# Kernel tuning notes

Measured on AMD Instinct MI355X. Metric: run time of the kernel, lower is better.

Reference implementation:

```python
import jax, jax.numpy as jnp
import numpy as np

N_NODES = 20000
DIM = 128
N_EDGES = 500000
BATCH = 16384
EPS = 1e-6  # torch.nn.PairwiseDistance default eps


def setup_inputs() -> dict:
    key = jax.random.key(0)
    k = jax.random.split(key, 8)
    edges = jax.random.randint(k[0], (2, N_EDGES), 0, N_NODES, dtype=jnp.int64 if jax.config.jax_enable_x64 else jnp.int32)
    nodes_p_star = jnp.sort(jax.random.randint(k[1], (BATCH,), 0, N_NODES))
    nodes_p = jnp.sort(jax.random.randint(k[2], (BATCH,), 0, N_NODES))
    # learned parameters, init in [-1, 1) as in the torch module
    beta_p = 2.0 * jax.random.uniform(k[3], (N_NODES,), dtype=jnp.float32) - 1.0
    beta_p_star = 2.0 * jax.random.uniform(k[4], (N_NODES,), dtype=jnp.float32) - 1.0
    p = 2.0 * jax.random.uniform(k[5], (N_NODES, DIM), dtype=jnp.float32) - 1.0
    p_star = 2.0 * jax.random.uniform(k[6], (N_NODES, DIM), dtype=jnp.float32) - 1.0
    return {
        "edges": edges,
        "nodes_p_star": nodes_p_star,
        "nodes_p": nodes_p,
        "beta_p": beta_p,
        "beta_p_star": beta_p_star,
        "p": p,
        "p_star": p_star,
    }


def reference(edges, nodes_p_star, nodes_p, beta_p, beta_p_star, p, p_star):
    # ---- link term: sum over observed edges of (beta - dist) ----
    beta_pair = beta_p_star[edges[0]] + beta_p[edges[1]]  # [E]
    diff = p[edges[0]] - p_star[edges[1]]                 # [E, D]
    # torch PairwiseDistance adds eps to the difference before the norm
    z_dist = jnp.sqrt(jnp.sum((diff + EPS) ** 2, axis=-1))
    link_term = jnp.sum(beta_pair - z_dist)

    # ---- non-link term: triu-masked sum of exp(beta - cdist) ----
    bps = beta_p_star[nodes_p_star]   # [Ns]
    bp = beta_p[nodes_p]              # [Np]
    ps = p_star[nodes_p_star]         # [Ns, D]
    pp = p[nodes_p]                   # [Np, D]
    beta_mat = bps[None, :] + bp[:, None]          # [Np, Ns]
    # cdist(ps, pp) -> [Ns, Np] via Gram trick
    sq = (jnp.sum(ps * ps, axis=-1)[:, None]
          + jnp.sum(pp * pp, axis=-1)[None, :]
          - 2.0 * jnp.einsum('nd,md->nm', ps, pp))
    dist_mat = jnp.sqrt(jnp.maximum(sq, 0.0))      # [Ns, Np]
    intensity = jnp.exp(beta_mat.T - dist_mat)     # [Ns, Np]
    non_link = jnp.sum(jnp.triu(intensity, k=1))

    return -(link_term - non_link)
```

## Files before the change

kernel.cpp:

```cpp
#include <hip/hip_runtime.h>
#include <hip/hip_bf16.h>

#define N_NODES 20000
#define DIM 128
#define N_EDGES 500000
#define BATCH 16384
#define EPS 1e-6f

typedef _Float16 half8 __attribute__((ext_vector_type(8)));
typedef _Float16 half4_t __attribute__((ext_vector_type(4)));
typedef float f32x4 __attribute__((ext_vector_type(4)));

__device__ __forceinline__ float fast_sqrtf(float x) {
#if __has_builtin(__builtin_amdgcn_sqrtf)
    return __builtin_amdgcn_sqrtf(x);
#else
    return sqrtf(x);
#endif
}

#define NB_GEMM 8256
#define NB_LINK16 31250
#define NB_LINK32 15625
#define NB_FIN  128

#define OFF_PGEMM 0
#define OFF_PLINK 33024
#define OFF_FPART 158080
#define OFF_PSH   158592
#define OFF_PPH   4352896
#define OFF_N2S   8547200
#define OFF_N2P   8612736
#define OFF_BPS   8678272
#define OFF_BP    8743808
#define OFF_BASE_END 8809344
#define OFF_P16   8809344
#define OFF_PS16  13929344
#define OFF_END   19049344

__global__ __launch_bounds__(256) void gather_kernel(
    const float* __restrict__ pts, const float* __restrict__ beta,
    const int* __restrict__ idx,
    _Float16* __restrict__ dst, float* __restrict__ n2, float* __restrict__ bdst)
{
    int g = threadIdx.x & 31;
    int row = blockIdx.x * 8 + (threadIdx.x >> 5);
    int id = idx[row];
    float4 v = ((const float4*)(pts + (size_t)id * DIM))[g];
    half4_t o;
    o[0] = (_Float16)v.x; o[1] = (_Float16)v.y; o[2] = (_Float16)v.z; o[3] = (_Float16)v.w;
    *(half4_t*)(dst + (size_t)row * DIM + g * 4) = o;
    float nrm = v.x * v.x + v.y * v.y + v.z * v.z + v.w * v.w;
    #pragma unroll
    for (int m = 16; m >= 1; m >>= 1) nrm += __shfl_xor(nrm, m, 32);
    if (g == 0) {
        n2[row] = nrm;
        bdst[row] = beta[id];
    }
}

__global__ __launch_bounds__(256) void convert_kernel(
    const float* __restrict__ src, _Float16* __restrict__ dst)
{
    int g = threadIdx.x & 31;
    int row = blockIdx.x * 8 + (threadIdx.x >> 5);
    float4 v = ((const float4*)(src + (size_t)row * DIM))[g];
    half4_t o;
    o[0] = (_Float16)v.x; o[1] = (_Float16)v.y; o[2] = (_Float16)v.z; o[3] = (_Float16)v.w;
    *(half4_t*)(dst + (size_t)row * DIM + g * 4) = o;
}

__global__ __launch_bounds__(256) void link16_kernel(
    const int* __restrict__ edges,
    const float* __restrict__ beta_p, const float* __restrict__ beta_ps,
    const _Float16* __restrict__ p16, const _Float16* __restrict__ ps16,
    float* __restrict__ partial)
{
    int g = threadIdx.x & 15;
    int grp = threadIdx.x >> 4;
    int e = blockIdx.x * 16 + grp;
    int e0 = edges[e];
    int e1 = edges[N_EDGES + e];
    half8 a = *(const half8*)(p16 + (size_t)e0 * DIM + g * 8);
    half8 b = *(const half8*)(ps16 + (size_t)e1 * DIM + g * 8);
    float s = 0.f;
    #pragma unroll
    for (int k = 0; k < 8; ++k) {
        float d = (float)a[k] - (float)b[k] + EPS;
        s = fmaf(d, d, s);
    }
    #pragma unroll
    for (int m = 8; m >= 1; m >>= 1) s += __shfl_xor(s, m, 16);
    __shared__ float sm[16];
    if (g == 0) {
        float bsum = beta_ps[e0] + beta_p[e1];
        sm[grp] = bsum - fast_sqrtf(s);
    }
    __syncthreads();
    if (threadIdx.x == 0) {
        float t = 0.f;
        #pragma unroll
        for (int i = 0; i < 16; ++i) t += sm[i];
        partial[blockIdx.x] = t;
    }
}

__global__ __launch_bounds__(256) void link32_kernel(
    const int* __restrict__ edges,
    const float* __restrict__ beta_p, const float* __restrict__ beta_ps,
    const float* __restrict__ p, const float* __restrict__ p_star,
    float* __restrict__ partial)
{
    int g = threadIdx.x & 31;
    int base = blockIdx.x * 32 + (threadIdx.x >> 5) * 4;
    float tacc = 0.f;
    #pragma unroll
    for (int t = 0; t < 4; ++t) {
        int e = base + t;
        int e0 = edges[e];
        int e1 = edges[N_EDGES + e];
        float4 a = ((const float4*)(p + (size_t)e0 * DIM))[g];
        float4 b = ((const float4*)(p_star + (size_t)e1 * DIM))[g];
        float dx = a.x - b.x + EPS;
        float dy = a.y - b.y + EPS;
        float dz = a.z - b.z + EPS;
        float dw = a.w - b.w + EPS;
        float s = dx * dx + dy * dy + dz * dz + dw * dw;
        #pragma unroll
        for (int m = 16; m >= 1; m >>= 1) s += __shfl_xor(s, m, 32);
        if (g == 0) tacc += (beta_ps[e0] + beta_p[e1]) - fast_sqrtf(s);
    }
    #pragma unroll
    for (int m = 32; m >= 1; m >>= 1) tacc += __shfl_xor(tacc, m, 64);
    __shared__ float sm[4];
    int w = threadIdx.x >> 6;
    if ((threadIdx.x & 63) == 0) sm[w] = tacc;
    __syncthreads();
    if (threadIdx.x == 0) partial[blockIdx.x] = sm[0] + sm[1] + sm[2] + sm[3];
}

__global__ __launch_bounds__(256) void nonlink_kernel(
    const _Float16* __restrict__ Ag, const _Float16* __restrict__ Bg,
    const float* __restrict__ n2A, const float* __restrict__ n2B,
    const float* __restrict__ bA, const float* __restrict__ bB,
    float* __restrict__ partial)
{
    const int bx = blockIdx.x, by = blockIdx.y;
    int ti, tj;
    if (bx >= by && bx < 128) { ti = by; tj = bx; }
    else { int u = (bx >= 128) ? by : bx; ti = 127 - by; tj = 127 - u; }
    const int i0 = ti * 128;
    const int j0 = tj * 128;
    const int bid = by * 129 + bx;
    const bool diag = (ti == tj);

    __shared__ __align__(16) _Float16 As[128][136];
    __shared__ __align__(16) _Float16 Bs[128][136];

    const int tid = threadIdx.x;
    #pragma unroll
    for (int c = tid; c < 2048; c += 256) {
        int row = c >> 4;
        int col = (c & 15) * 8;
        *(uint4*)&As[row][col] = *(const uint4*)(Ag + (size_t)(i0 + row) * DIM + col);
        *(uint4*)&Bs[row][col] = *(const uint4*)(Bg + (size_t)(j0 + row) * DIM + col);
    }
    __syncthreads();

    const int lane = tid & 63;
    const int w = tid >> 6;
    const int wm = w & 1;
    const int wn = w >> 1;
    const int quad = lane >> 4;
    const int lr = lane & 15;

    float lsum = 0.f;
    const bool dead = diag && (wm > wn);
    if (!dead) {
        f32x4 acc[4][4] = {};
        #pragma unroll
        for (int ks = 0; ks < 4; ++ks) {
            int koff = ks * 32 + quad * 8;
            half8 af[4], bf[4];
            #pragma unroll
            for (int t = 0; t < 4; ++t) {
                af[t] = *(const half8*)&As[wm * 64 + t * 16 + lr][koff];
                bf[t] = *(const half8*)&Bs[wn * 64 + t * 16 + lr][koff];
            }
            #pragma unroll
            for (int mi = 0; mi < 4; ++mi)
                #pragma unroll
                for (int ni = 0; ni < 4; ++ni)
                    acc[mi][ni] = __builtin_amdgcn_mfma_f32_16x16x32_f16(af[mi], bf[ni], acc[mi][ni], 0, 0, 0);
        }

        const bool masked = diag && (wm == wn);
        #pragma unroll
        for (int mi = 0; mi < 4; ++mi) {
            int rbase = wm * 64 + mi * 16 + quad * 4;
            float4 n2i = *(const float4*)&n2A[i0 + rbase];
            float4 bi = *(const float4*)&bA[i0 + rbase];
            #pragma unroll
            for (int ni = 0; ni < 4; ++ni) {
                int jc = wn * 64 + ni * 16 + lr;
                float n2j = n2B[j0 + jc];
                float bj = bB[j0 + jc];
                f32x4 d = acc[mi][ni];
                #pragma unroll
                for (int r = 0; r < 4; ++r) {
                    float sq = fmaxf(((const float*)&n2i)[r] + n2j - 2.f * d[r], 0.f);
                    float dist = fast_sqrtf(sq);
                    float ex = __expf(((const float*)&bi)[r] + bj - dist);
                    if (!masked || jc > rbase + r) lsum += ex;
                }
            }
        }
    }

    #pragma unroll
    for (int m = 32; m >= 1; m >>= 1) lsum += __shfl_xor(lsum, m, 64);
    __shared__ float smr[4];
    if (lane == 0) smr[w] = lsum;
    __syncthreads();
    if (tid == 0) partial[bid] = smr[0] + smr[1] + smr[2] + smr[3];
}

__global__ __launch_bounds__(256) void reduce1_kernel(
    const float* __restrict__ pg, const float* __restrict__ pl, int nlink,
    float* __restrict__ fpart)
{
    float s = 0.f;
    for (int k = blockIdx.x * 256 + threadIdx.x; k < NB_GEMM; k += NB_FIN * 256) s += pg[k];
    for (int k = blockIdx.x * 256 + threadIdx.x; k < nlink; k += NB_FIN * 256) s -= pl[k];
    #pragma unroll
    for (int m = 32; m >= 1; m >>= 1) s += __shfl_xor(s, m, 64);
    __shared__ float sm[4];
    int w = threadIdx.x >> 6;
    if ((threadIdx.x & 63) == 0) sm[w] = s;
    __syncthreads();
    if (threadIdx.x == 0) fpart[blockIdx.x] = sm[0] + sm[1] + sm[2] + sm[3];
}

__global__ __launch_bounds__(128) void reduce2_kernel(
    const float* __restrict__ fpart, float* __restrict__ out)
{
    float s = fpart[threadIdx.x];
    #pragma unroll
    for (int m = 32; m >= 1; m >>= 1) s += __shfl_xor(s, m, 64);
    __shared__ float sm[2];
    if ((threadIdx.x & 63) == 0) sm[threadIdx.x >> 6] = s;
    __syncthreads();
    if (threadIdx.x == 0) out[0] = sm[0] + sm[1];
}

extern "C" void kernel_launch(void* const* d_in, const int* in_sizes, int n_in,
                              void* d_out, int out_size, void* d_ws, size_t ws_size,
                              hipStream_t stream) {
    const int* edges = (const int*)d_in[0];
    const int* nodes_p_star = (const int*)d_in[1];
    const int* nodes_p = (const int*)d_in[2];
    const float* beta_p = (const float*)d_in[3];
    const float* beta_p_star = (const float*)d_in[4];
    const float* p = (const float*)d_in[5];
    const float* p_star = (const float*)d_in[6];

    char* ws = (char*)d_ws;
    float* pgemm = (float*)(ws + OFF_PGEMM);
    float* plink = (float*)(ws + OFF_PLINK);
    float* fpart = (float*)(ws + OFF_FPART);
    _Float16* psh = (_Float16*)(ws + OFF_PSH);
    _Float16* pph = (_Float16*)(ws + OFF_PPH);
    float* n2s = (float*)(ws + OFF_N2S);
    float* n2p = (float*)(ws + OFF_N2P);
    float* bps = (float*)(ws + OFF_BPS);
    float* bp = (float*)(ws + OFF_BP);

    gather_kernel<<<BATCH / 8, 256, 0, stream>>>(p_star, beta_p_star, nodes_p_star, psh, n2s, bps);
    gather_kernel<<<BATCH / 8, 256, 0, stream>>>(p, beta_p, nodes_p, pph, n2p, bp);

    const bool use16 = ws_size >= (size_t)OFF_END;
    int nlink;
    if (use16) {
        _Float16* p16 = (_Float16*)(ws + OFF_P16);
        _Float16* ps16 = (_Float16*)(ws + OFF_PS16);
        convert_kernel<<<N_NODES / 8, 256, 0, stream>>>(p, p16);
        convert_kernel<<<N_NODES / 8, 256, 0, stream>>>(p_star, ps16);
        link16_kernel<<<NB_LINK16, 256, 0, stream>>>(edges, beta_p, beta_p_star, p16, ps16, plink);
        nlink = NB_LINK16;
    } else {
        link32_kernel<<<NB_LINK32, 256, 0, stream>>>(edges, beta_p, beta_p_star, p, p_star, plink);
        nlink = NB_LINK32;
    }

    nonlink_kernel<<<dim3(129, 64), 256, 0, stream>>>(psh, pph, n2s, n2p, bps, bp, pgemm);

    reduce1_kernel<<<NB_FIN, 256, 0, stream>>>(pgemm, plink, nlink, fpart);
    reduce2_kernel<<<1, 128, 0, stream>>>(fpart, (float*)d_out);
}
```

Before: 211.9 us.

## Fuse link and nonlink into one interleaved kernel with 128x64 tiles

Merges the two gather launches and two convert launches into a single prep kernel. The link-edge kernel and the triangular Gram/exp kernel are fused into one launch that interleaves one link block after every four 128x64 tile blocks, so memory-bound and compute-bound work overlap. Tiles shrink to 128x64 for finer triangular coverage, fully-upper warps skip the mask check, and exp is rewritten as exp2 with log2(e) prescaled into beta. The cost is a larger unified kernel whose register/LDS footprint applies to the link blocks as well.

```diff
diff --git a/kernel.cpp b/kernel.cpp
--- a/kernel.cpp
+++ b/kernel.cpp
@@ -6,6 +6,7 @@
 #define N_EDGES 500000
 #define BATCH 16384
 #define EPS 1e-6f
+#define L2E 1.4426950408889634f
 
 typedef _Float16 half8 __attribute__((ext_vector_type(8)));
 typedef _Float16 half4_t __attribute__((ext_vector_type(4)));
@@ -18,154 +19,149 @@
     return sqrtf(x);
 #endif
 }
-
-#define NB_GEMM 8256
-#define NB_LINK16 31250
-#define NB_LINK32 15625
-#define NB_FIN  128
+__device__ __forceinline__ float fast_exp2f(float x) {
+#if __has_builtin(__builtin_amdgcn_exp2f)
+    return __builtin_amdgcn_exp2f(x);
+#else
+    return exp2f(x);
+#endif
+}
+
+#define NB_TILE 16512
+#define NB_LINKB 4128
+#define NB_MAIN 20640
+#define LINK_EPB 128
+#define NB_FIN 128
 
 #define OFF_PGEMM 0
-#define OFF_PLINK 33024
-#define OFF_FPART 158080
-#define OFF_PSH   158592
-#define OFF_PPH   4352896
-#define OFF_N2S   8547200
-#define OFF_N2P   8612736
-#define OFF_BPS   8678272
-#define OFF_BP    8743808
-#define OFF_BASE_END 8809344
-#define OFF_P16   8809344
-#define OFF_PS16  13929344
-#define OFF_END   19049344
-
-__global__ __launch_bounds__(256) void gather_kernel(
-    const float* __restrict__ pts, const float* __restrict__ beta,
-    const int* __restrict__ idx,
-    _Float16* __restrict__ dst, float* __restrict__ n2, float* __restrict__ bdst)
+#define OFF_PLINK 66048
+#define OFF_FPART 82560
+#define OFF_PSH   83072
+#define OFF_PPH   4277376
+#define OFF_N2S   8471680
+#define OFF_N2P   8537216
+#define OFF_BPS   8602752
+#define OFF_BP    8668288
+#define OFF_P16   8733824
+#define OFF_PS16  13853824
+#define OFF_END   18973824
+
+__global__ __launch_bounds__(256) void prep_kernel(
+    const float* __restrict__ p, const float* __restrict__ p_star,
+    const float* __restrict__ beta_p, const float* __restrict__ beta_ps,
+    const int* __restrict__ nodes_ps, const int* __restrict__ nodes_p,
+    _Float16* __restrict__ Ah, float* __restrict__ n2A, float* __restrict__ bA2,
+    _Float16* __restrict__ Bh, float* __restrict__ n2B, float* __restrict__ bB2,
+    _Float16* __restrict__ p16, _Float16* __restrict__ ps16)
 {
-    int g = threadIdx.x & 31;
-    int row = blockIdx.x * 8 + (threadIdx.x >> 5);
-    int id = idx[row];
-    float4 v = ((const float4*)(pts + (size_t)id * DIM))[g];
-    half4_t o;
-    o[0] = (_Float16)v.x; o[1] = (_Float16)v.y; o[2] = (_Float16)v.z; o[3] = (_Float16)v.w;
-    *(half4_t*)(dst + (size_t)row * DIM + g * 4) = o;
-    float nrm = v.x * v.x + v.y * v.y + v.z * v.z + v.w * v.w;
-    #pragma unroll
-    for (int m = 16; m >= 1; m >>= 1) nrm += __shfl_xor(nrm, m, 32);
-    if (g == 0) {
-        n2[row] = nrm;
-        bdst[row] = beta[id];
-    }
-}
-
-__global__ __launch_bounds__(256) void convert_kernel(
-    const float* __restrict__ src, _Float16* __restrict__ dst)
-{
-    int g = threadIdx.x & 31;
-    int row = blockIdx.x * 8 + (threadIdx.x >> 5);
-    float4 v = ((const float4*)(src + (size_t)row * DIM))[g];
-    half4_t o;
-    o[0] = (_Float16)v.x; o[1] = (_Float16)v.y; o[2] = (_Float16)v.z; o[3] = (_Float16)v.w;
-    *(half4_t*)(dst + (size_t)row * DIM + g * 4) = o;
-}
-
-__global__ __launch_bounds__(256) void link16_kernel(
+    const int bx = blockIdx.x;
+    const int g = threadIdx.x & 31;
+    const int r8 = threadIdx.x >> 5;
+    if (bx < 4096) {
+        const bool isA = bx < 2048;
+        int row = (isA ? bx : bx - 2048) * 8 + r8;
+        int id = isA ? nodes_ps[row] : nodes_p[row];
+        const float* src = isA ? p_star : p;
+        float4 v = ((const float4*)(src + (size_t)id * DIM))[g];
+        half4_t o;
+        o[0] = (_Float16)v.x; o[1] = (_Float16)v.y; o[2] = (_Float16)v.z; o[3] = (_Float16)v.w;
+        _Float16* dst = isA ? Ah : Bh;
+        *(half4_t*)(dst + (size_t)row * DIM + g * 4) = o;
+        float nrm = v.x * v.x + v.y * v.y + v.z * v.z + v.w * v.w;
+        #pragma unroll
+        for (int m = 16; m >= 1; m >>= 1) nrm += __shfl_xor(nrm, m, 32);
+        if (g == 0) {
+            if (isA) { n2A[row] = nrm; bA2[row] = L2E * beta_ps[id]; }
+            else     { n2B[row] = nrm; bB2[row] = L2E * beta_p[id]; }
+        }
+    } else {
+        const bool isP = bx < 6596;
+        int row = (isP ? bx - 4096 : bx - 6596) * 8 + r8;
+        const float* src = isP ? p : p_star;
+        _Float16* dst = isP ? p16 : ps16;
+        float4 v = ((const float4*)(src + (size_t)row * DIM))[g];
+        half4_t o;
+        o[0] = (_Float16)v.x; o[1] = (_Float16)v.y; o[2] = (_Float16)v.z; o[3] = (_Float16)v.w;
+        *(half4_t*)(dst + (size_t)row * DIM + g * 4) = o;
+    }
+}
+
+__global__ __launch_bounds__(256) void main_kernel(
+    const _Float16* __restrict__ Ag, const _Float16* __restrict__ Bg,
+    const float* __restrict__ n2A, const float* __restrict__ n2B,
+    const float* __restrict__ bA2, const float* __restrict__ bB2,
     const int* __restrict__ edges,
     const float* __restrict__ beta_p, const float* __restrict__ beta_ps,
     const _Float16* __restrict__ p16, const _Float16* __restrict__ ps16,
-    float* __restrict__ partial)
+    const float* __restrict__ pf, const float* __restrict__ psf, int use16,
+    float* __restrict__ pgemm, float* __restrict__ plink)
 {
-    int g = threadIdx.x & 15;
-    int grp = threadIdx.x >> 4;
-    int e = blockIdx.x * 16 + grp;
-    int e0 = edges[e];
-    int e1 = edges[N_EDGES + e];
-    half8 a = *(const half8*)(p16 + (size_t)e0 * DIM + g * 8);
-    half8 b = *(const half8*)(ps16 + (size_t)e1 * DIM + g * 8);
-    float s = 0.f;
-    #pragma unroll
-    for (int k = 0; k < 8; ++k) {
-        float d = (float)a[k] - (float)b[k] + EPS;
-        s = fmaf(d, d, s);
-    }
-    #pragma unroll
-    for (int m = 8; m >= 1; m >>= 1) s += __shfl_xor(s, m, 16);
-    __shared__ float sm[16];
-    if (g == 0) {
-        float bsum = beta_ps[e0] + beta_p[e1];
-        sm[grp] = bsum - fast_sqrtf(s);
-    }
-    __syncthreads();
-    if (threadIdx.x == 0) {
-        float t = 0.f;
+    const int f = blockIdx.x;
+    const int grp5 = f / 5, rem5 = f % 5;
+    const int tid = threadIdx.x;
+
+    __shared__ __align__(16) _Float16 As[128][136];
+    __shared__ __align__(16) _Float16 Bs[64][136];
+    __shared__ float smr[4];
+
+    if (rem5 == 4) {
+        float tacc = 0.f;
+        if (use16) {
+            int g = tid & 15, grp = tid >> 4;
+            #pragma unroll
+            for (int t = 0; t < 8; ++t) {
+                int e = grp5 * LINK_EPB + t * 16 + grp;
+                if (e < N_EDGES) {
+                    int e0 = edges[e];
+                    int e1 = edges[N_EDGES + e];
+                    half8 a = *(const half8*)(p16 + (size_t)e0 * DIM + g * 8);
+                    half8 b = *(const half8*)(ps16 + (size_t)e1 * DIM + g * 8);
+                    float s = 0.f;
+                    #pragma unroll
+                    for (int k = 0; k < 8; ++k) {
+                        float d = (float)a[k] - (float)b[k] + EPS;
+                        s = fmaf(d, d, s);
+                    }
+                    #pragma unroll
+                    for (int m = 8; m >= 1; m >>= 1) s += __shfl_xor(s, m, 16);
+                    if (g == 0) tacc += (beta_ps[e0] + beta_p[e1]) - fast_sqrtf(s);
+                }
+            }
+        } else {
+            int g = tid & 31, grp = tid >> 5;
+            #pragma unroll
+            for (int t = 0; t < 16; ++t) {
+                int e = grp5 * LINK_EPB + t * 8 + grp;
+                if (e < N_EDGES) {
+                    int e0 = edges[e];
+                    int e1 = edges[N_EDGES + e];
+                    float4 a = ((const float4*)(pf + (size_t)e0 * DIM))[g];
+                    float4 b = ((const float4*)(psf + (size_t)e1 * DIM))[g];
+                    float dx = a.x - b.x + EPS, dy = a.y - b.y + EPS;
+                    float dz = a.z - b.z + EPS, dw = a.w - b.w + EPS;
+                    float s = dx * dx + dy * dy + dz * dz + dw * dw;
+                    #pragma unroll
+                    for (int m = 16; m >= 1; m >>= 1) s += __shfl_xor(s, m, 32);
+                    if (g == 0) tacc += (beta_ps[e0] + beta_p[e1]) - fast_sqrtf(s);
+                }
+            }
+        }
         #pragma unroll
-        for (int i = 0; i < 16; ++i) t += sm[i];
-        partial[blockIdx.x] = t;
-    }
-}
-
-__global__ __launch_bounds__(256) void link32_kernel(
-    const int* __restrict__ edges,
-    const float* __restrict__ beta_p, const float* __restrict__ beta_ps,
-    const float* __restrict__ p, const float* __restrict__ p_star,
-    float* __restrict__ partial)
-{
-    int g = threadIdx.x & 31;
-    int base = blockIdx.x * 32 + (threadIdx.x >> 5) * 4;
-    float tacc = 0.f;
-    #pragma unroll
-    for (int t = 0; t < 4; ++t) {
-        int e = base + t;
-        int e0 = edges[e];
-        int e1 = edges[N_EDGES + e];
-        float4 a = ((const float4*)(p + (size_t)e0 * DIM))[g];
-        float4 b = ((const float4*)(p_star + (size_t)e1 * DIM))[g];
-        float dx = a.x - b.x + EPS;
-        float dy = a.y - b.y + EPS;
-        float dz = a.z - b.z + EPS;
-        float dw = a.w - b.w + EPS;
-        float s = dx * dx + dy * dy + dz * dz + dw * dw;
-        #pragma unroll
-        for (int m = 16; m >= 1; m >>= 1) s += __shfl_xor(s, m, 32);
-        if (g == 0) tacc += (beta_ps[e0] + beta_p[e1]) - fast_sqrtf(s);
-    }
-    #pragma unroll
-    for (int m = 32; m >= 1; m >>= 1) tacc += __shfl_xor(tacc, m, 64);
-    __shared__ float sm[4];
-    int w = threadIdx.x >> 6;
-    if ((threadIdx.x & 63) == 0) sm[w] = tacc;
-    __syncthreads();
-    if (threadIdx.x == 0) partial[blockIdx.x] = sm[0] + sm[1] + sm[2] + sm[3];
-}
-
-__global__ __launch_bounds__(256) void nonlink_kernel(
-    const _Float16* __restrict__ Ag, const _Float16* __restrict__ Bg,
-    const float* __restrict__ n2A, const float* __restrict__ n2B,
-    const float* __restrict__ bA, const float* __restrict__ bB,
-    float* __restrict__ partial)
-{
-    const int bx = blockIdx.x, by = blockIdx.y;
+        for (int m = 32; m >= 1; m >>= 1) tacc += __shfl_xor(tacc, m, 64);
+        if ((tid & 63) == 0) smr[tid >> 6] = tacc;
+        __syncthreads();
+        if (tid == 0) plink[grp5] = smr[0] + smr[1] + smr[2] + smr[3];
+        return;
+    }
+
+    const int t = grp5 * 4 + rem5;
+    const int by = t / 258, bx = t % 258;
     int ti, tj;
-    if (bx >= by && bx < 128) { ti = by; tj = bx; }
-    else { int u = (bx >= 128) ? by : bx; ti = 127 - by; tj = 127 - u; }
+    const int len = 256 - 2 * by;
+    if (bx < len) { ti = by; tj = 2 * by + bx; }
+    else          { ti = 127 - by; tj = bx - 2; }
     const int i0 = ti * 128;
-    const int j0 = tj * 128;
-    const int bid = by * 129 + bx;
-    const bool diag = (ti == tj);
-
-    __shared__ __align__(16) _Float16 As[128][136];
-    __shared__ __align__(16) _Float16 Bs[128][136];
-
-    const int tid = threadIdx.x;
-    #pragma unroll
-    for (int c = tid; c < 2048; c += 256) {
-        int row = c >> 4;
-        int col = (c & 15) * 8;
-        *(uint4*)&As[row][col] = *(const uint4*)(Ag + (size_t)(i0 + row) * DIM + col);
-        *(uint4*)&Bs[row][col] = *(const uint4*)(Bg + (size_t)(j0 + row) * DIM + col);
-    }
-    __syncthreads();
+    const int j0 = tj * 64;
 
     const int lane = tid & 63;
     const int w = tid >> 6;
@@ -173,65 +169,102 @@
     const int wn = w >> 1;
     const int quad = lane >> 4;
     const int lr = lane & 15;
+    const int ilo = i0 + wm * 64;
+    const int jlo = j0 + wn * 32;
+
+    float4 n2i[4], bi[4];
+    float n2j[2], bj[2];
+    #pragma unroll
+    for (int mi = 0; mi < 4; ++mi) {
+        n2i[mi] = *(const float4*)&n2A[ilo + mi * 16 + quad * 4];
+        bi[mi] = *(const float4*)&bA2[ilo + mi * 16 + quad * 4];
+    }
+    #pragma unroll
+    for (int ni = 0; ni < 2; ++ni) {
+        n2j[ni] = n2B[jlo + ni * 16 + lr];
+        bj[ni] = bB2[jlo + ni * 16 + lr];
+    }
+
+    #pragma unroll
+    for (int c = tid; c < 2048; c += 256)
+        *(uint4*)&As[c >> 4][(c & 15) * 8] =
+            *(const uint4*)(Ag + (size_t)(i0 + (c >> 4)) * DIM + (c & 15) * 8);
+    #pragma unroll
+    for (int c = tid; c < 1024; c += 256)
+        *(uint4*)&Bs[c >> 4][(c & 15) * 8] =
+            *(const uint4*)(Bg + (size_t)(j0 + (c >> 4)) * DIM + (c & 15) * 8);
+    __syncthreads();
+
+    const bool dead = (jlo + 31 <= ilo);
+    const bool freew = (jlo > ilo + 63);
 
     float lsum = 0.f;
-    const bool dead = diag && (wm > wn);
     if (!dead) {
-        f32x4 acc[4][4] = {};
+        f32x4 acc[4][2] = {};
         #pragma unroll
         for (int ks = 0; ks < 4; ++ks) {
             int koff = ks * 32 + quad * 8;
-            half8 af[4], bf[4];
-            #pragma unroll
-            for (int t = 0; t < 4; ++t) {
-                af[t] = *(const half8*)&As[wm * 64 + t * 16 + lr][koff];
-                bf[t] = *(const half8*)&Bs[wn * 64 + t * 16 + lr][koff];
-            }
+            half8 af[4], bf[2];
+            #pragma unroll
+            for (int u = 0; u < 4; ++u) af[u] = *(const half8*)&As[wm * 64 + u * 16 + lr][koff];
+            #pragma unroll
+            for (int u = 0; u < 2; ++u) bf[u] = *(const half8*)&Bs[wn * 32 + u * 16 + lr][koff];
             #pragma unroll
             for (int mi = 0; mi < 4; ++mi)
                 #pragma unroll
-                for (int ni = 0; ni < 4; ++ni)
+                for (int ni = 0; ni < 2; ++ni)
                     acc[mi][ni] = __builtin_amdgcn_mfma_f32_16x16x32_f16(af[mi], bf[ni], acc[mi][ni], 0, 0, 0);
         }
 
-        const bool masked = diag && (wm == wn);
-        #pragma unroll
-        for (int mi = 0; mi < 4; ++mi) {
-            int rbase = wm * 64 + mi * 16 + quad * 4;
-            float4 n2i = *(const float4*)&n2A[i0 + rbase];
-            float4 bi = *(const float4*)&bA[i0 + rbase];
-            #pragma unroll
-            for (int ni = 0; ni < 4; ++ni) {
-                int jc = wn * 64 + ni * 16 + lr;
-                float n2j = n2B[j0 + jc];
-                float bj = bB[j0 + jc];
-                f32x4 d = acc[mi][ni];
+        if (freew) {
+            #pragma unroll
+            for (int mi = 0; mi < 4; ++mi)
                 #pragma unroll
-                for (int r = 0; r < 4; ++r) {
-                    float sq = fmaxf(((const float*)&n2i)[r] + n2j - 2.f * d[r], 0.f);
-                    float dist = fast_sqrtf(sq);
-                    float ex = __expf(((const float*)&bi)[r] + bj - dist);
-                    if (!masked || jc > rbase + r) lsum += ex;
+                for (int ni = 0; ni < 2; ++ni) {
+                    f32x4 d = acc[mi][ni];
+                    #pragma unroll
+                    for (int r = 0; r < 4; ++r) {
+                        float tt = ((const float*)&n2i[mi])[r] + n2j[ni];
+                        float sq = fmaxf(fmaf(d[r], -2.f, tt), 0.f);
+                        float dist = fast_sqrtf(sq);
+                        float arg = fmaf(dist, -L2E, ((const float*)&bi[mi])[r] + bj[ni]);
+                        lsum += fast_exp2f(arg);
+                    }
                 }
-            }
+        } else {
+            #pragma unroll
+            for (int mi = 0; mi < 4; ++mi)
+                #pragma unroll
+                for (int ni = 0; ni < 2; ++ni) {
+                    f32x4 d = acc[mi][ni];
+                    #pragma unroll
+                    for (int r = 0; r < 4; ++r) {
+                        int ig = ilo + mi * 16 + quad * 4 + r;
+                        int jg = jlo + ni * 16 + lr;
+                        float tt = ((const float*)&n2i[mi])[r] + n2j[ni];
+                        float sq = fmaxf(fmaf(d[r], -2.f, tt), 0.f);
+                        float dist = fast_sqrtf(sq);
+                        float arg = fmaf(dist, -L2E, ((const float*)&bi[mi])[r] + bj[ni]);
+                        float ex = fast_exp2f(arg);
+                        if (jg > ig) lsum += ex;
+                    }
+                }
         }
     }
 
     #pragma unroll
     for (int m = 32; m >= 1; m >>= 1) lsum += __shfl_xor(lsum, m, 64);
-    __shared__ float smr[4];
     if (lane == 0) smr[w] = lsum;
     __syncthreads();
-    if (tid == 0) partial[bid] = smr[0] + smr[1] + smr[2] + smr[3];
+    if (tid == 0) pgemm[t] = smr[0] + smr[1] + smr[2] + smr[3];
 }
 
 __global__ __launch_bounds__(256) void reduce1_kernel(
-    const float* __restrict__ pg, const float* __restrict__ pl, int nlink,
-    float* __restrict__ fpart)
+    const float* __restrict__ pg, const float* __restrict__ pl, float* __restrict__ fpart)
 {
     float s = 0.f;
-    for (int k = blockIdx.x * 256 + threadIdx.x; k < NB_GEMM; k += NB_FIN * 256) s += pg[k];
-    for (int k = blockIdx.x * 256 + threadIdx.x; k < nlink; k += NB_FIN * 256) s -= pl[k];
+    for (int k = blockIdx.x * 256 + threadIdx.x; k < NB_TILE; k += NB_FIN * 256) s += pg[k];
+    for (int k = blockIdx.x * 256 + threadIdx.x; k < NB_LINKB; k += NB_FIN * 256) s -= pl[k];
     #pragma unroll
     for (int m = 32; m >= 1; m >>= 1) s += __shfl_xor(s, m, 64);
     __shared__ float sm[4];
@@ -272,28 +305,22 @@
     _Float16* pph = (_Float16*)(ws + OFF_PPH);
     float* n2s = (float*)(ws + OFF_N2S);
     float* n2p = (float*)(ws + OFF_N2P);
-    float* bps = (float*)(ws + OFF_BPS);
-    float* bp = (float*)(ws + OFF_BP);
-
-    gather_kernel<<<BATCH / 8, 256, 0, stream>>>(p_star, beta_p_star, nodes_p_star, psh, n2s, bps);
-    gather_kernel<<<BATCH / 8, 256, 0, stream>>>(p, beta_p, nodes_p, pph, n2p, bp);
-
-    const bool use16 = ws_size >= (size_t)OFF_END;
-    int nlink;
-    if (use16) {
-        _Float16* p16 = (_Float16*)(ws + OFF_P16);
-        _Float16* ps16 = (_Float16*)(ws + OFF_PS16);
-        convert_kernel<<<N_NODES / 8, 256, 0, stream>>>(p, p16);
-        convert_kernel<<<N_NODES / 8, 256, 0, stream>>>(p_star, ps16);
-        link16_kernel<<<NB_LINK16, 256, 0, stream>>>(edges, beta_p, beta_p_star, p16, ps16, plink);
-        nlink = NB_LINK16;
-    } else {
-        link32_kernel<<<NB_LINK32, 256, 0, stream>>>(edges, beta_p, beta_p_star, p, p_star, plink);
-        nlink = NB_LINK32;
-    }
-
-    nonlink_kernel<<<dim3(129, 64), 256, 0, stream>>>(psh, pph, n2s, n2p, bps, bp, pgemm);
-
-    reduce1_kernel<<<NB_FIN, 256, 0, stream>>>(pgemm, plink, nlink, fpart);
+    float* bps2 = (float*)(ws + OFF_BPS);
+    float* bp2 = (float*)(ws + OFF_BP);
+    _Float16* p16 = (_Float16*)(ws + OFF_P16);
+    _Float16* ps16 = (_Float16*)(ws + OFF_PS16);
+
+    const int use16 = (ws_size >= (size_t)OFF_END) ? 1 : 0;
+
+    prep_kernel<<<9096, 256, 0, stream>>>(
+        p, p_star, beta_p, beta_p_star, nodes_p_star, nodes_p,
+        psh, n2s, bps2, pph, n2p, bp2, p16, ps16);
+
+    main_kernel<<<NB_MAIN, 256, 0, stream>>>(
+        psh, pph, n2s, n2p, bps2, bp2,
+        edges, beta_p, beta_p_star, p16, ps16, p, p_star, use16,
+        pgemm, plink);
+
+    reduce1_kernel<<<NB_FIN, 256, 0, stream>>>(pgemm, plink, fpart);
     reduce2_kernel<<<1, 128, 0, stream>>>(fpart, (float*)d_out);
 }
```

After: 237.5 us. 12.1% more time.
